# Performance work log

Hardware: AMD Instinct MI355X
Metric: run time of the kernel (lower is better)

Reference implementation:

```python
import jax, jax.numpy as jnp
import numpy as np

BSZ, SEQ, HID = 8, 4096, 1024
N_EXPERTS = 8
CAPACITY = 512  # expert_capacity_per_batch; effective cap = min(SEQ, CAPACITY)
SCALE = 1.0     # routed_scaling_factor


def setup_inputs() -> dict:
    key = jax.random.key(0)
    k1, k2 = jax.random.split(key)
    hidden_states = jax.random.normal(k1, (BSZ, SEQ, HID), dtype=jnp.float32)
    # kaiming_uniform_(a=sqrt(5)) on [d,e] -> bound = 1/sqrt(fan_in=d)
    bound = 1.0 / np.sqrt(HID)
    weight = jax.random.uniform(k2, (HID, N_EXPERTS), dtype=jnp.float32,
                                minval=-bound, maxval=bound)
    return {"hidden_states": hidden_states, "weight": weight}


def reference(hidden_states, weight):
    bsz, seq_len, h = hidden_states.shape
    # gating logits in fp32: [b, s, e]
    logits = jnp.einsum('bsd,de->bse', hidden_states.astype(jnp.float32),
                        weight.astype(jnp.float32))
    affinity = jax.nn.softmax(logits, axis=-1)          # [b, s, e]
    affinity = jnp.transpose(affinity, (0, 2, 1))       # [b, e, s]
    cap = min(seq_len, CAPACITY)                        # static
    # Each expert picks its top-`cap` tokens (sorted descending, like torch.topk)
    topk_scores, topk_indices = jax.lax.top_k(affinity, cap)  # [b, e, cap]
    topk_scores = topk_scores * SCALE
    # dense dispatch mask [b, e, cap, s]: one-hot over token positions
    dispatch_mask = jax.nn.one_hot(topk_indices, seq_len, dtype=jnp.float32)
    return topk_indices, topk_scores, dispatch_mask
```

## Files before the change

### kernel.cpp

```cpp
#include <hip/hip_runtime.h>

constexpr int BSZ = 8, SEQ = 4096, HID = 1024, NE = 8, CAP = 512;
constexpr int ROWS = BSZ * NE;
constexpr size_t IDX_ELEMS = (size_t)ROWS * CAP;
constexpr size_t SCR_OFF = IDX_ELEMS;
constexpr size_t MASK_OFF = IDX_ELEMS * 2;
constexpr size_t MASK_ELEMS = (size_t)ROWS * CAP * SEQ;
constexpr size_t AFF_ELEMS = (size_t)ROWS * SEQ;
constexpr size_t AFF_BYTES = AFF_ELEMS * sizeof(float);
constexpr size_t KEYS_BYTES = (size_t)ROWS * SEQ * 8;

constexpr long long NZ4_TOTAL = (long long)(MASK_ELEMS >> 2);

typedef float f4v __attribute__((ext_vector_type(4)));

__global__ __launch_bounds__(128) void gatezero_kernel(const float* __restrict__ hidden,
                                                       const float* __restrict__ weight,
                                                       float* __restrict__ aff,
                                                       float* __restrict__ out)
{
    __shared__ float hls[16][68];
    __shared__ float wls[8][68];
    __shared__ float lls[16][8];

    if (blockIdx.x >= 2048) {
        f4v* mz = (f4v*)(out + MASK_OFF);
        const f4v z4 = {0.f, 0.f, 0.f, 0.f};
        const long long stride = (long long)(gridDim.x - 2048) * 128;
        for (long long i = (long long)(blockIdx.x - 2048) * 128 + threadIdx.x;
             i < NZ4_TOTAL; i += stride)
            __builtin_nontemporal_store(z4, mz + i);
        return;
    }

    const int tid = threadIdx.x;
    const int T0 = blockIdx.x * 16;
    const int t = tid >> 3;
    const int e = tid & 7;

    float v0 = 0.f, v1 = 0.f, v2 = 0.f, v3 = 0.f;
    for (int c = 0; c < 16; ++c) {
        __syncthreads();
#pragma unroll
        for (int k = 0; k < 2; ++k) {
            const int j = tid + k * 128;
            const int tt = j >> 4, q = j & 15;
            const float4 v = *(const float4*)(hidden + (size_t)(T0 + tt) * HID + c * 64 + 4 * q);
            *(float4*)&hls[tt][4 * q] = v;
        }
#pragma unroll
        for (int k = 0; k < 4; ++k) {
            const int j = tid + k * 128;
            const int dd = j >> 3, ee = j & 7;
            wls[ee][dd] = weight[(size_t)(c * 64 + dd) * NE + ee];
        }
        __syncthreads();
#pragma unroll
        for (int k = 0; k < 4; ++k) {
            const int base = 16 * k;
            const float4 hA = *(const float4*)&hls[t][base + 0];
            const float4 hB = *(const float4*)&hls[t][base + 4];
            const float4 hC = *(const float4*)&hls[t][base + 8];
            const float4 hD = *(const float4*)&hls[t][base + 12];
            const float4 wA = *(const float4*)&wls[e][base + 0];
            const float4 wB = *(const float4*)&wls[e][base + 4];
            const float4 wC = *(const float4*)&wls[e][base + 8];
            const float4 wD = *(const float4*)&wls[e][base + 12];
            v0 = __fadd_rn(__fmul_rn(hA.x, wA.x),
                 __fadd_rn(__fmul_rn(hB.x, wB.x),
                 __fadd_rn(__fmul_rn(hC.x, wC.x),
                 __fadd_rn(__fmul_rn(hD.x, wD.x), v0))));
            v1 = __fadd_rn(__fmul_rn(hA.y, wA.y),
                 __fadd_rn(__fmul_rn(hB.y, wB.y),
                 __fadd_rn(__fmul_rn(hC.y, wC.y),
                 __fadd_rn(__fmul_rn(hD.y, wD.y), v1))));
            v2 = __fadd_rn(__fmul_rn(hA.z, wA.z),
                 __fadd_rn(__fmul_rn(hB.z, wB.z),
                 __fadd_rn(__fmul_rn(hC.z, wC.z),
                 __fadd_rn(__fmul_rn(hD.z, wD.z), v2))));
            v3 = __fadd_rn(__fmul_rn(hA.w, wA.w),
                 __fadd_rn(__fmul_rn(hB.w, wB.w),
                 __fadd_rn(__fmul_rn(hC.w, wC.w),
                 __fadd_rn(__fmul_rn(hD.w, wD.w), v3))));
        }
    }
    const float logit = __fadd_rn(__fadd_rn(v0, v1), __fadd_rn(v2, v3));

    lls[t][e] = logit;
    __syncthreads();

    float l[8];
#pragma unroll
    for (int k = 0; k < 8; ++k) l[k] = lls[t][k];
    float m = l[0];
#pragma unroll
    for (int k = 1; k < 8; ++k) m = fmaxf(m, l[k]);
    float p[8];
#pragma unroll
    for (int k = 0; k < 8; ++k)
        p[k] = (float)exp((double)__fsub_rn(l[k], m));
    const float s = __fadd_rn(__fadd_rn(__fadd_rn(p[0], p[1]), __fadd_rn(p[2], p[3])),
                              __fadd_rn(__fadd_rn(p[4], p[5]), __fadd_rn(p[6], p[7])));
    const float a = __fdiv_rn(p[e], s);

    const int token = T0 + t;
    const int b = token >> 12;
    const int sidx = token & (SEQ - 1);
    aff[((size_t)b * NE + e) * SEQ + sidx] = a;
}

__global__ __launch_bounds__(256) void segsort_kernel(const float* __restrict__ aff,
                                                      unsigned long long* __restrict__ keys)
{
    __shared__ unsigned long long k[512];
    const int row = blockIdx.x >> 3, seg = blockIdx.x & 7;
    const int g0 = seg * 512;
    const float* a = aff + (size_t)row * SEQ + g0;
    for (int j = threadIdx.x; j < 512; j += 256) {
        const unsigned int fb = __float_as_uint(a[j]);
        k[j] = ((unsigned long long)fb << 32) | (unsigned int)(SEQ - 1 - (g0 + j));
    }
    for (int len = 2; len <= 512; len <<= 1) {
        for (int stride = len >> 1; stride > 0; stride >>= 1) {
            __syncthreads();
            const int t = threadIdx.x;
            const int i = (t << 1) - (t & (stride - 1));
            const int j = i + stride;
            const unsigned long long ki = k[i], kj = k[j];
            const bool desc = ((i & len) == 0);
            if (desc ? (ki < kj) : (ki > kj)) { k[i] = kj; k[j] = ki; }
        }
    }
    __syncthreads();
    unsigned long long* dst = keys + (size_t)row * SEQ + g0;
    for (int j = threadIdx.x; j < 512; j += 256) dst[j] = k[j];
}

__global__ __launch_bounds__(512) void merge_scatter_kernel(const unsigned long long* __restrict__ keys,
                                                            float* __restrict__ out)
{
    __shared__ unsigned long long A[SEQ];
    const int row = blockIdx.x;
    for (int i = threadIdx.x; i < SEQ; i += 512)
        A[i] = keys[(size_t)row * SEQ + i];

    for (int round = 0; round < 3; ++round) {
        const int sp = 1024 << round;
        const int npairs = 4 >> round;
        __syncthreads();
        for (int u = threadIdx.x; u < npairs * 512; u += 512) {
            const int p = u >> 9, i = u & 511;
            const int base = p * sp;
            const unsigned long long x = A[base + i];
            const unsigned long long y = A[base + sp / 2 + 511 - i];
            if (y > x) A[base + i] = y;
        }
        for (int s = 256; s > 0; s >>= 1) {
            __syncthreads();
            for (int u = threadIdx.x; u < npairs * 256; u += 512) {
                const int r = u >> 8, t2 = u & 255;
                const int base = r * sp;
                const int i = (t2 << 1) - (t2 & (s - 1));
                const unsigned long long x = A[base + i], y = A[base + i + s];
                if (y > x) { A[base + i] = y; A[base + i + s] = x; }
            }
        }
    }
    __syncthreads();
    if (threadIdx.x < CAP) {
        const int t = threadIdx.x;
        const unsigned long long k = A[t];
        const int idx = (SEQ - 1) - (int)(unsigned int)(k & 0xffffffffu);
        out[(size_t)row * CAP + t] = (float)idx;
        out[SCR_OFF + (size_t)row * CAP + t] =
            __uint_as_float((unsigned int)(k >> 32));
        out[MASK_OFF + ((size_t)row * CAP + t) * SEQ + idx] = 1.0f;
    }
}

__global__ __launch_bounds__(128) void gating_kernel(const float* __restrict__ hidden,
                                                     const float* __restrict__ weight,
                                                     float* __restrict__ aff)
{
    __shared__ float hls[16][68];
    __shared__ float wls[8][68];
    __shared__ float lls[16][8];

    const int tid = threadIdx.x;
    const int T0 = blockIdx.x * 16;
    const int t = tid >> 3;
    const int e = tid & 7;

    float v0 = 0.f, v1 = 0.f, v2 = 0.f, v3 = 0.f;
    for (int c = 0; c < 16; ++c) {
        __syncthreads();
#pragma unroll
        for (int k = 0; k < 2; ++k) {
            const int j = tid + k * 128;
            const int tt = j >> 4, q = j & 15;
            const float4 v = *(const float4*)(hidden + (size_t)(T0 + tt) * HID + c * 64 + 4 * q);
            *(float4*)&hls[tt][4 * q] = v;
        }
#pragma unroll
        for (int k = 0; k < 4; ++k) {
            const int j = tid + k * 128;
            const int dd = j >> 3, ee = j & 7;
            wls[ee][dd] = weight[(size_t)(c * 64 + dd) * NE + ee];
        }
        __syncthreads();
#pragma unroll
        for (int k = 0; k < 4; ++k) {
            const int base = 16 * k;
            const float4 hA = *(const float4*)&hls[t][base + 0];
            const float4 hB = *(const float4*)&hls[t][base + 4];
            const float4 hC = *(const float4*)&hls[t][base + 8];
            const float4 hD = *(const float4*)&hls[t][base + 12];
            const float4 wA = *(const float4*)&wls[e][base + 0];
            const float4 wB = *(const float4*)&wls[e][base + 4];
            const float4 wC = *(const float4*)&wls[e][base + 8];
            const float4 wD = *(const float4*)&wls[e][base + 12];
            v0 = __fadd_rn(__fmul_rn(hA.x, wA.x),
                 __fadd_rn(__fmul_rn(hB.x, wB.x),
                 __fadd_rn(__fmul_rn(hC.x, wC.x),
                 __fadd_rn(__fmul_rn(hD.x, wD.x), v0))));
            v1 = __fadd_rn(__fmul_rn(hA.y, wA.y),
                 __fadd_rn(__fmul_rn(hB.y, wB.y),
                 __fadd_rn(__fmul_rn(hC.y, wC.y),
                 __fadd_rn(__fmul_rn(hD.y, wD.y), v1))));
            v2 = __fadd_rn(__fmul_rn(hA.z, wA.z),
                 __fadd_rn(__fmul_rn(hB.z, wB.z),
                 __fadd_rn(__fmul_rn(hC.z, wC.z),
                 __fadd_rn(__fmul_rn(hD.z, wD.z), v2))));
            v3 = __fadd_rn(__fmul_rn(hA.w, wA.w),
                 __fadd_rn(__fmul_rn(hB.w, wB.w),
                 __fadd_rn(__fmul_rn(hC.w, wC.w),
                 __fadd_rn(__fmul_rn(hD.w, wD.w), v3))));
        }
    }
    const float logit = __fadd_rn(__fadd_rn(v0, v1), __fadd_rn(v2, v3));

    lls[t][e] = logit;
    __syncthreads();

    float l[8];
#pragma unroll
    for (int k = 0; k < 8; ++k) l[k] = lls[t][k];
    float m = l[0];
#pragma unroll
    for (int k = 1; k < 8; ++k) m = fmaxf(m, l[k]);
    float p[8];
#pragma unroll
    for (int k = 0; k < 8; ++k)
        p[k] = (float)exp((double)__fsub_rn(l[k], m));
    const float s = __fadd_rn(__fadd_rn(__fadd_rn(p[0], p[1]), __fadd_rn(p[2], p[3])),
                              __fadd_rn(__fadd_rn(p[4], p[5]), __fadd_rn(p[6], p[7])));
    const float a = __fdiv_rn(p[e], s);

    const int token = T0 + t;
    const int b = token >> 12;
    const int sidx = token & (SEQ - 1);
    aff[((size_t)b * NE + e) * SEQ + sidx] = a;
}

__global__ __launch_bounds__(1024) void sortzero_kernel(const float* __restrict__ aff,
                                                        float* __restrict__ out)
{
    __shared__ unsigned long long keys[SEQ];
    const int row = blockIdx.x;
    const float* a = aff + (size_t)row * SEQ;
    float* mrow = out + MASK_OFF + (size_t)row * CAP * SEQ;

    for (int i = threadIdx.x; i < SEQ; i += 1024) {
        const unsigned int fb = __float_as_uint(a[i]);
        keys[i] = ((unsigned long long)fb << 32) | (unsigned int)(SEQ - 1 - i);
    }
    f4v* mz = (f4v*)mrow;
    const f4v z4 = {0.f, 0.f, 0.f, 0.f};
    int zi = 0;
    for (int len = 2; len <= SEQ; len <<= 1) {
        for (int stride = len >> 1; stride > 0; stride >>= 1) {
            __syncthreads();
#pragma unroll
            for (int k = 0; k < 7; ++k) {
                if (zi < 512) {
                    __builtin_nontemporal_store(z4, mz + (size_t)zi * 1024 + threadIdx.x);
                    ++zi;
                }
            }
            for (int t = threadIdx.x; t < SEQ / 2; t += 1024) {
                const int i = (t << 1) - (t & (stride - 1));
                const int j = i + stride;
                const unsigned long long ki = keys[i], kj = keys[j];
                const bool desc = ((i & len) == 0);
                if (desc ? (ki < kj) : (ki > kj)) { keys[i] = kj; keys[j] = ki; }
            }
        }
    }
    __syncthreads();
    if (threadIdx.x < CAP) {
        const int t = threadIdx.x;
        const unsigned long long k = keys[t];
        const int idx = (SEQ - 1) - (int)(unsigned int)(k & 0xffffffffu);
        out[(size_t)row * CAP + t] = (float)idx;
        out[SCR_OFF + (size_t)row * CAP + t] =
            __uint_as_float((unsigned int)(k >> 32));
        mrow[(size_t)t * SEQ + idx] = 1.0f;
    }
}

__global__ __launch_bounds__(1024) void topk_zero_kernel(const float* __restrict__ aff,
                                                         float* __restrict__ out,
                                                         long long zero_elems)
{
    __shared__ unsigned long long keys[SEQ];
    if (blockIdx.x < (unsigned)ROWS) {
        const int row = blockIdx.x;
        const float* a = aff + (size_t)row * SEQ;
        for (int i = threadIdx.x; i < SEQ; i += 1024) {
            const unsigned int fb = __float_as_uint(a[i]);
            keys[i] = ((unsigned long long)fb << 32) | (unsigned int)(SEQ - 1 - i);
        }
        for (int len = 2; len <= SEQ; len <<= 1) {
            for (int stride = len >> 1; stride > 0; stride >>= 1) {
                __syncthreads();
                for (int t = threadIdx.x; t < SEQ / 2; t += 1024) {
                    const int i = (t << 1) - (t & (stride - 1));
                    const int j = i + stride;
                    const unsigned long long ki = keys[i], kj = keys[j];
                    const bool desc = ((i & len) == 0);
                    if (desc ? (ki < kj) : (ki > kj)) { keys[i] = kj; keys[j] = ki; }
                }
            }
        }
        __syncthreads();
        if (threadIdx.x < CAP) {
            const int t = threadIdx.x;
            const unsigned long long k = keys[t];
            const int idx = (SEQ - 1) - (int)(unsigned int)(k & 0xffffffffu);
            out[(size_t)row * CAP + t] = (float)idx;
            out[SCR_OFF + (size_t)row * CAP + t] =
                __uint_as_float((unsigned int)(k >> 32));
        }
    } else {
        const long long nz4 = zero_elems >> 2;
        f4v* mz = (f4v*)(out + MASK_OFF);
        const f4v z4 = {0.f, 0.f, 0.f, 0.f};
        const long long stride = (long long)(gridDim.x - ROWS) * 1024;
        for (long long i = (long long)(blockIdx.x - ROWS) * 1024 + threadIdx.x;
             i < nz4; i += stride)
            __builtin_nontemporal_store(z4, mz + i);
    }
}

__global__ void tailzero_kernel(float* __restrict__ out)
{
    const long long n4 = (long long)(AFF_ELEMS >> 2);
    f4v* mz = (f4v*)(out + MASK_OFF + MASK_ELEMS - AFF_ELEMS);
    const f4v z4 = {0.f, 0.f, 0.f, 0.f};
    const long long i = (long long)blockIdx.x * blockDim.x + threadIdx.x;
    if (i < n4) __builtin_nontemporal_store(z4, mz + i);
}

__global__ void scatter_kernel(float* __restrict__ out)
{
    const int p = blockIdx.x * blockDim.x + threadIdx.x;
    if (p < (int)IDX_ELEMS) {
        const int idx = (int)out[p];
        out[MASK_OFF + (size_t)p * SEQ + idx] = 1.0f;
    }
}

extern "C" void kernel_launch(void* const* d_in, const int* in_sizes, int n_in,
                              void* d_out, int out_size, void* d_ws, size_t ws_size,
                              hipStream_t stream)
{
    const float* hidden = (const float*)d_in[0];
    const float* weight = (const float*)d_in[1];
    float* out = (float*)d_out;

    if (ws_size >= AFF_BYTES + KEYS_BYTES) {
        float* aff = (float*)d_ws;
        unsigned long long* keys = (unsigned long long*)((char*)d_ws + AFF_BYTES);
        gatezero_kernel<<<2048 + 1920, 128, 0, stream>>>(hidden, weight, aff, out);
        segsort_kernel<<<512, 256, 0, stream>>>(aff, keys);
        merge_scatter_kernel<<<ROWS, 512, 0, stream>>>(keys, out);
    } else if (ws_size >= AFF_BYTES) {
        float* aff = (float*)d_ws;
        gating_kernel<<<2048, 128, 0, stream>>>(hidden, weight, aff);
        sortzero_kernel<<<ROWS, 1024, 0, stream>>>(aff, out);
    } else {
        float* aff = out + MASK_OFF + MASK_ELEMS - AFF_ELEMS;
        gating_kernel<<<2048, 128, 0, stream>>>(hidden, weight, aff);
        const long long zero_elems = (long long)(MASK_ELEMS - AFF_ELEMS);
        topk_zero_kernel<<<ROWS + 1984, 1024, 0, stream>>>(aff, out, zero_elems);
        tailzero_kernel<<<256, 256, 0, stream>>>(out);
        scatter_kernel<<<(int)((IDX_ELEMS + 255) / 256), 256, 0, stream>>>(out);
    }
}
```

Baseline: 659.0 us.

## Fuse segment sort and merge into one kernel that overlaps mask zeroing

```diff
diff --git a/kernel.cpp b/kernel.cpp
--- a/kernel.cpp
+++ b/kernel.cpp
@@ -8,9 +8,9 @@
 constexpr size_t MASK_ELEMS = (size_t)ROWS * CAP * SEQ;
 constexpr size_t AFF_ELEMS = (size_t)ROWS * SEQ;
 constexpr size_t AFF_BYTES = AFF_ELEMS * sizeof(float);
-constexpr size_t KEYS_BYTES = (size_t)ROWS * SEQ * 8;
 
 constexpr long long NZ4_TOTAL = (long long)(MASK_ELEMS >> 2);
+constexpr long long Z_SPLIT   = NZ4_TOTAL * 5 / 8;
 
 typedef float f4v __attribute__((ext_vector_type(4)));
 
@@ -28,7 +28,7 @@
         const f4v z4 = {0.f, 0.f, 0.f, 0.f};
         const long long stride = (long long)(gridDim.x - 2048) * 128;
         for (long long i = (long long)(blockIdx.x - 2048) * 128 + threadIdx.x;
-             i < NZ4_TOTAL; i += stride)
+             i < Z_SPLIT; i += stride)
             __builtin_nontemporal_store(z4, mz + i);
         return;
     }
@@ -109,72 +109,77 @@
     aff[((size_t)b * NE + e) * SEQ + sidx] = a;
 }
 
-__global__ __launch_bounds__(256) void segsort_kernel(const float* __restrict__ aff,
-                                                      unsigned long long* __restrict__ keys)
-{
-    __shared__ unsigned long long k[512];
-    const int row = blockIdx.x >> 3, seg = blockIdx.x & 7;
-    const int g0 = seg * 512;
-    const float* a = aff + (size_t)row * SEQ + g0;
-    for (int j = threadIdx.x; j < 512; j += 256) {
-        const unsigned int fb = __float_as_uint(a[j]);
-        k[j] = ((unsigned long long)fb << 32) | (unsigned int)(SEQ - 1 - (g0 + j));
-    }
-    for (int len = 2; len <= 512; len <<= 1) {
-        for (int stride = len >> 1; stride > 0; stride >>= 1) {
+__global__ __launch_bounds__(512) void sortmerge_zero_kernel(const float* __restrict__ aff,
+                                                             float* __restrict__ out)
+{
+    __shared__ unsigned long long A[SEQ];
+    if (blockIdx.x < (unsigned)ROWS) {
+        const int row = blockIdx.x;
+        const float* a = aff + (size_t)row * SEQ;
+        for (int i = threadIdx.x; i < SEQ; i += 512) {
+            const unsigned int fb = __float_as_uint(a[i]);
+            A[i] = ((unsigned long long)fb << 32) | (unsigned int)(SEQ - 1 - i);
+        }
+        for (int len = 2; len <= 512; len <<= 1) {
+            for (int stride = len >> 1; stride > 0; stride >>= 1) {
+                __syncthreads();
+                for (int u = threadIdx.x; u < 2048; u += 512) {
+                    const int seg = u >> 8, t2 = u & 255;
+                    const int i = (t2 << 1) - (t2 & (stride - 1));
+                    const int gi = seg * 512 + i, gj = gi + stride;
+                    const unsigned long long ki = A[gi], kj = A[gj];
+                    const bool desc = ((i & len) == 0);
+                    if (desc ? (ki < kj) : (ki > kj)) { A[gi] = kj; A[gj] = ki; }
+                }
+            }
+        }
+        for (int round = 0; round < 3; ++round) {
+            const int sp = 1024 << round;
+            const int npairs = 4 >> round;
             __syncthreads();
+            for (int u = threadIdx.x; u < npairs * 512; u += 512) {
+                const int p = u >> 9, i = u & 511;
+                const int base = p * sp;
+                const unsigned long long x = A[base + i];
+                const unsigned long long y = A[base + sp / 2 + 511 - i];
+                if (y > x) A[base + i] = y;
+            }
+            for (int s = 256; s > 0; s >>= 1) {
+                __syncthreads();
+                for (int u = threadIdx.x; u < npairs * 256; u += 512) {
+                    const int r = u >> 8, t2 = u & 255;
+                    const int base = r * sp;
+                    const int i = (t2 << 1) - (t2 & (s - 1));
+                    const unsigned long long x = A[base + i], y = A[base + i + s];
+                    if (y > x) { A[base + i] = y; A[base + i + s] = x; }
+                }
+            }
+        }
+        __syncthreads();
+        if (threadIdx.x < CAP) {
             const int t = threadIdx.x;
-            const int i = (t << 1) - (t & (stride - 1));
-            const int j = i + stride;
-            const unsigned long long ki = k[i], kj = k[j];
-            const bool desc = ((i & len) == 0);
-            if (desc ? (ki < kj) : (ki > kj)) { k[i] = kj; k[j] = ki; }
-        }
-    }
-    __syncthreads();
-    unsigned long long* dst = keys + (size_t)row * SEQ + g0;
-    for (int j = threadIdx.x; j < 512; j += 256) dst[j] = k[j];
-}
-
-__global__ __launch_bounds__(512) void merge_scatter_kernel(const unsigned long long* __restrict__ keys,
-                                                            float* __restrict__ out)
-{
-    __shared__ unsigned long long A[SEQ];
-    const int row = blockIdx.x;
-    for (int i = threadIdx.x; i < SEQ; i += 512)
-        A[i] = keys[(size_t)row * SEQ + i];
-
-    for (int round = 0; round < 3; ++round) {
-        const int sp = 1024 << round;
-        const int npairs = 4 >> round;
-        __syncthreads();
-        for (int u = threadIdx.x; u < npairs * 512; u += 512) {
-            const int p = u >> 9, i = u & 511;
-            const int base = p * sp;
-            const unsigned long long x = A[base + i];
-            const unsigned long long y = A[base + sp / 2 + 511 - i];
-            if (y > x) A[base + i] = y;
-        }
-        for (int s = 256; s > 0; s >>= 1) {
-            __syncthreads();
-            for (int u = threadIdx.x; u < npairs * 256; u += 512) {
-                const int r = u >> 8, t2 = u & 255;
-                const int base = r * sp;
-                const int i = (t2 << 1) - (t2 & (s - 1));
-                const unsigned long long x = A[base + i], y = A[base + i + s];
-                if (y > x) { A[base + i] = y; A[base + i + s] = x; }
-            }
-        }
-    }
-    __syncthreads();
-    if (threadIdx.x < CAP) {
-        const int t = threadIdx.x;
-        const unsigned long long k = A[t];
-        const int idx = (SEQ - 1) - (int)(unsigned int)(k & 0xffffffffu);
-        out[(size_t)row * CAP + t] = (float)idx;
-        out[SCR_OFF + (size_t)row * CAP + t] =
-            __uint_as_float((unsigned int)(k >> 32));
-        out[MASK_OFF + ((size_t)row * CAP + t) * SEQ + idx] = 1.0f;
+            const unsigned long long k = A[t];
+            const int idx = (SEQ - 1) - (int)(unsigned int)(k & 0xffffffffu);
+            out[(size_t)row * CAP + t] = (float)idx;
+            out[SCR_OFF + (size_t)row * CAP + t] =
+                __uint_as_float((unsigned int)(k >> 32));
+        }
+    } else {
+        f4v* mz = (f4v*)(out + MASK_OFF);
+        const f4v z4 = {0.f, 0.f, 0.f, 0.f};
+        const long long stride = (long long)(gridDim.x - ROWS) * 512;
+        for (long long i = Z_SPLIT + (long long)(blockIdx.x - ROWS) * 512 + threadIdx.x;
+             i < NZ4_TOTAL; i += stride)
+            __builtin_nontemporal_store(z4, mz + i);
+    }
+}
+
+__global__ void scatter_kernel(float* __restrict__ out)
+{
+    const int p = blockIdx.x * blockDim.x + threadIdx.x;
+    if (p < (int)IDX_ELEMS) {
+        const int idx = (int)out[p];
+        out[MASK_OFF + (size_t)p * SEQ + idx] = 1.0f;
     }
 }
 
@@ -262,52 +267,6 @@
     aff[((size_t)b * NE + e) * SEQ + sidx] = a;
 }
 
-__global__ __launch_bounds__(1024) void sortzero_kernel(const float* __restrict__ aff,
-                                                        float* __restrict__ out)
-{
-    __shared__ unsigned long long keys[SEQ];
-    const int row = blockIdx.x;
-    const float* a = aff + (size_t)row * SEQ;
-    float* mrow = out + MASK_OFF + (size_t)row * CAP * SEQ;
-
-    for (int i = threadIdx.x; i < SEQ; i += 1024) {
-        const unsigned int fb = __float_as_uint(a[i]);
-        keys[i] = ((unsigned long long)fb << 32) | (unsigned int)(SEQ - 1 - i);
-    }
-    f4v* mz = (f4v*)mrow;
-    const f4v z4 = {0.f, 0.f, 0.f, 0.f};
-    int zi = 0;
-    for (int len = 2; len <= SEQ; len <<= 1) {
-        for (int stride = len >> 1; stride > 0; stride >>= 1) {
-            __syncthreads();
-#pragma unroll
-            for (int k = 0; k < 7; ++k) {
-                if (zi < 512) {
-                    __builtin_nontemporal_store(z4, mz + (size_t)zi * 1024 + threadIdx.x);
-                    ++zi;
-                }
-            }
-            for (int t = threadIdx.x; t < SEQ / 2; t += 1024) {
-                const int i = (t << 1) - (t & (stride - 1));
-                const int j = i + stride;
-                const unsigned long long ki = keys[i], kj = keys[j];
-                const bool desc = ((i & len) == 0);
-                if (desc ? (ki < kj) : (ki > kj)) { keys[i] = kj; keys[j] = ki; }
-            }
-        }
-    }
-    __syncthreads();
-    if (threadIdx.x < CAP) {
-        const int t = threadIdx.x;
-        const unsigned long long k = keys[t];
-        const int idx = (SEQ - 1) - (int)(unsigned int)(k & 0xffffffffu);
-        out[(size_t)row * CAP + t] = (float)idx;
-        out[SCR_OFF + (size_t)row * CAP + t] =
-            __uint_as_float((unsigned int)(k >> 32));
-        mrow[(size_t)t * SEQ + idx] = 1.0f;
-    }
-}
-
 __global__ __launch_bounds__(1024) void topk_zero_kernel(const float* __restrict__ aff,
                                                          float* __restrict__ out,
                                                          long long zero_elems)
@@ -361,15 +320,6 @@
     if (i < n4) __builtin_nontemporal_store(z4, mz + i);
 }
 
-__global__ void scatter_kernel(float* __restrict__ out)
-{
-    const int p = blockIdx.x * blockDim.x + threadIdx.x;
-    if (p < (int)IDX_ELEMS) {
-        const int idx = (int)out[p];
-        out[MASK_OFF + (size_t)p * SEQ + idx] = 1.0f;
-    }
-}
-
 extern "C" void kernel_launch(void* const* d_in, const int* in_sizes, int n_in,
                               void* d_out, int out_size, void* d_ws, size_t ws_size,
                               hipStream_t stream)
@@ -378,16 +328,11 @@
     const float* weight = (const float*)d_in[1];
     float* out = (float*)d_out;
 
-    if (ws_size >= AFF_BYTES + KEYS_BYTES) {
+    if (ws_size >= AFF_BYTES) {
         float* aff = (float*)d_ws;
-        unsigned long long* keys = (unsigned long long*)((char*)d_ws + AFF_BYTES);
         gatezero_kernel<<<2048 + 1920, 128, 0, stream>>>(hidden, weight, aff, out);
-        segsort_kernel<<<512, 256, 0, stream>>>(aff, keys);
-        merge_scatter_kernel<<<ROWS, 512, 0, stream>>>(keys, out);
-    } else if (ws_size >= AFF_BYTES) {
-        float* aff = (float*)d_ws;
-        gating_kernel<<<2048, 128, 0, stream>>>(hidden, weight, aff);
-        sortzero_kernel<<<ROWS, 1024, 0, stream>>>(aff, out);
+        sortmerge_zero_kernel<<<ROWS + 960, 512, 0, stream>>>(aff, out);
+        scatter_kernel<<<(int)((IDX_ELEMS + 255) / 256), 256, 0, stream>>>(out);
     } else {
         float* aff = out + MASK_OFF + MASK_ELEMS - AFF_ELEMS;
         gating_kernel<<<2048, 128, 0, stream>>>(hidden, weight, aff);
```

New measurement: 636.9 us. -3.4%, faster.
